# Kernel optimization log

Hardware: AMD Instinct MI355X
Metric: run time of the kernel (lower is better)

## Reference

```python
import jax, jax.numpy as jnp
import numpy as np
from jax import lax

B, T, P, H, O = 64, 96, 256, 128, 24  # batch, seq_len, num_points, hidden_dim, pred_len


def setup_inputs() -> dict:
    key = jax.random.key(0)
    ks = jax.random.split(key, 7)
    s = 1.0 / np.sqrt(H)  # torch LSTM/Linear default init scale
    return {
        "x": jax.random.normal(ks[0], (B, T, P, 1), dtype=jnp.float32),
        "W_ih": jax.random.uniform(ks[1], (P, 4 * H, 1), jnp.float32, -s, s),
        "W_hh": jax.random.uniform(ks[2], (P, 4 * H, H), jnp.float32, -s, s),
        "b_ih": jax.random.uniform(ks[3], (P, 4 * H), jnp.float32, -s, s),
        "b_hh": jax.random.uniform(ks[4], (P, 4 * H), jnp.float32, -s, s),
        "W_fc": jax.random.uniform(ks[5], (P, O, H), jnp.float32, -s, s),
        "b_fc": jax.random.uniform(ks[6], (P, O), jnp.float32, -s, s),
    }


def reference(x, W_ih, W_hh, b_ih, b_hh, W_fc, b_fc):
    # x: [B, T, P, F]; model uses only feature 0
    xs = x[..., 0]  # [B, T, P]
    # input_dim == 1, so input-to-gate contribution is a scaled broadcast of W_ih
    # precompute for all timesteps: [T, B, P, 4H]
    gx = jnp.einsum("btp,pg->tbpg", xs, W_ih[:, :, 0]) + (b_ih + b_hh)

    def step(carry, gxt):
        h, c = carry  # [B, P, H] each
        gates = gxt + jnp.einsum("bph,pgh->bpg", h, W_hh)  # [B, P, 4H]
        i, f, g, o = jnp.split(gates, 4, axis=-1)  # torch gate order i,f,g,o
        i = jax.nn.sigmoid(i)
        f = jax.nn.sigmoid(f)
        g = jnp.tanh(g)
        o = jax.nn.sigmoid(o)
        c = f * c + i * g
        h = o * jnp.tanh(c)
        return (h, c), None

    h0 = jnp.zeros((B, P, H), dtype=x.dtype)
    (h, _), _ = lax.scan(step, (h0, h0), gx)
    # per-point Linear on final hidden state: [B, P, O]
    out = jnp.einsum("bph,poh->bpo", h, W_fc) + b_fc
    # original stacks point outputs on last dim -> [B, pred_len, P]
    return jnp.transpose(out, (0, 2, 1))
```

## Files before the change

kernel.cpp:

```cpp
#include <hip/hip_runtime.h>
#include <hip/hip_bf16.h>

#define Bdim 64
#define Tdim 96
#define Pdim 256
#define Hdim 128
#define Gdim 512
#define Odim 24
#define BH   32

typedef _Float16 f16x8 __attribute__((ext_vector_type(8)));
typedef float    f32x16 __attribute__((ext_vector_type(16)));
typedef float    f32x2  __attribute__((ext_vector_type(2)));

union H8 { uint4 u4; unsigned short s[8]; _Float16 h[8]; f16x8 v; };
union HS { _Float16 h; unsigned short s; };

__device__ __forceinline__ float exp2_fast(float x) {
#if __has_builtin(__builtin_amdgcn_exp2f)
    return __builtin_amdgcn_exp2f(x);
#else
    return __expf(x * 0.6931471805599453f);
#endif
}

__global__ __launch_bounds__(1024, 4)
void lstm_fused(const float* __restrict__ x,
                const float* __restrict__ W_ih,
                const float* __restrict__ W_hh,
                const float* __restrict__ b_ih,
                const float* __restrict__ b_hh,
                const float* __restrict__ W_fc,
                const float* __restrict__ b_fc,
                float* __restrict__ out)
{
    __shared__ unsigned short hb0[2][BH * Hdim];
    __shared__ unsigned short hb1[2][BH * Hdim];

    const int p   = blockIdx.x;
    const int tid = threadIdx.x;
    const int w   = tid >> 6;
    const int l31 = tid & 31;
    const int hi  = (tid >> 5) & 1;

    const float L1 = 1.4426950408889634f;
    const float L2 = 2.0f * L1;

    for (int i = tid; i < 2 * BH * Hdim; i += 1024) ((unsigned short*)hb0)[i] = 0;
    for (int i = tid; i < 2 * BH * Hdim; i += 1024) ((unsigned short*)hb1)[i] = 0;

    f16x8 afr[9];
    {
        const int rp   = w * 32 + l31;
        const int orow = ((rp & 3) << 7) | (rp >> 2);
        const float sc = ((rp & 3) == 2) ? L2 : L1;
        const float* rowp = W_hh + (size_t)p * Gdim * Hdim + (size_t)orow * Hdim;
        #pragma unroll
        for (int ks = 0; ks < 8; ++ks) {
            int k0 = ks * 16 + hi * 8;
            float4 va = *(const float4*)(rowp + k0);
            float4 vb = *(const float4*)(rowp + k0 + 4);
            H8 u;
            u.h[0] = (_Float16)(sc * va.x); u.h[1] = (_Float16)(sc * va.y);
            u.h[2] = (_Float16)(sc * va.z); u.h[3] = (_Float16)(sc * va.w);
            u.h[4] = (_Float16)(sc * vb.x); u.h[5] = (_Float16)(sc * vb.y);
            u.h[6] = (_Float16)(sc * vb.z); u.h[7] = (_Float16)(sc * vb.w);
            afr[ks] = u.v;
        }
        H8 u9;
        #pragma unroll
        for (int j = 0; j < 8; ++j) u9.s[j] = 0;
        if (hi == 0) {
            u9.h[0] = (_Float16)(sc * W_ih[(size_t)p * Gdim + orow]);
            u9.h[1] = (_Float16)(sc * (b_ih[(size_t)p * Gdim + orow] +
                                       b_hh[(size_t)p * Gdim + orow]));
        }
        afr[8] = u9.v;
    }

    auto ldh = [&](const unsigned short* hb, int ks) -> H8 {
        H8 r;
        int c   = ks * 2 + hi;
        int off = (l31 << 8) + ((c ^ (l31 & 15)) << 4);
        r.u4 = *(const uint4*)((const char*)hb + off);
        return r;
    };

    auto ep_pair = [&](const f32x16& a, int j, f32x2* cr, unsigned short* wb) {
        f32x2 yi = {a[8 * j + 0], a[8 * j + 4]};
        f32x2 yf = {a[8 * j + 1], a[8 * j + 5]};
        f32x2 yg = {a[8 * j + 2], a[8 * j + 6]};
        f32x2 yo = {a[8 * j + 3], a[8 * j + 7]};
        f32x2 Ef = {exp2_fast(-yf.x), exp2_fast(-yf.y)};
        f32x2 Ei = {exp2_fast(-yi.x), exp2_fast(-yi.y)};
        f32x2 Eg = {exp2_fast(yg.x),  exp2_fast(yg.y)};
        f32x2 t1 = Ef + 1.0f;
        f32x2 t2 = Ei + 1.0f;
        f32x2 t3 = Eg + 1.0f;
        f32x2 t4 = Eg - 1.0f;
        f32x2 den = (t1 * t2) * t3;
        f32x2 num = (cr[j] * t2) * t3 + (L2 * t4) * t1;
        float D = den.x * den.y;
        float r = __builtin_amdgcn_rcpf(D);
        f32x2 inv = {r * den.y, r * den.x};
        f32x2 cn  = num * inv;
        cn.x = __builtin_amdgcn_fmed3f(cn.x, -30.0f, 30.0f);
        cn.y = __builtin_amdgcn_fmed3f(cn.y, -30.0f, 30.0f);
        cr[j] = cn;
        f32x2 Eo = {exp2_fast(-yo.x), exp2_fast(-yo.y)};
        f32x2 Ec = {exp2_fast(cn.x),  exp2_fast(cn.y)};
        f32x2 d2 = (Eo + 1.0f) * (Ec + 1.0f);
        float D2 = d2.x * d2.y;
        float r2 = __builtin_amdgcn_rcpf(D2);
        f32x2 j2 = {r2 * d2.y, r2 * d2.x};
        f32x2 hv = (Ec - 1.0f) * j2;
        HS ha; ha.h = (_Float16)hv.x;
        HS hc; hc.h = (_Float16)hv.y;
        int base = (l31 << 7) + ((w ^ (l31 & 15)) << 3) + 4 * j + hi;
        wb[base]     = ha.s;
        wb[base + 2] = hc.s;
    };

    auto phase = [&](const unsigned short* rb, unsigned short* wb,
                     f32x16& acc, const f32x16& ar, f32x2* cr, float xv,
                     bool doGemm, bool doEp) {
        if (doGemm) {
            H8 f0 = ldh(rb, 0), f1 = ldh(rb, 1);
            H8 f2 = ldh(rb, 2), f3 = ldh(rb, 3);
            f32x16 z;
            #pragma unroll
            for (int j = 0; j < 16; ++j) z[j] = 0.f;
            acc = __builtin_amdgcn_mfma_f32_32x32x16_f16(afr[0], f0.v, z, 0, 0, 0);
            acc = __builtin_amdgcn_mfma_f32_32x32x16_f16(afr[1], f1.v, acc, 0, 0, 0);
            if (doEp) ep_pair(ar, 0, cr, wb);
            H8 f4 = ldh(rb, 4), f5 = ldh(rb, 5);
            acc = __builtin_amdgcn_mfma_f32_32x32x16_f16(afr[2], f2.v, acc, 0, 0, 0);
            acc = __builtin_amdgcn_mfma_f32_32x32x16_f16(afr[3], f3.v, acc, 0, 0, 0);
            if (doEp) ep_pair(ar, 1, cr, wb);
            H8 f6 = ldh(rb, 6), f7 = ldh(rb, 7);
            acc = __builtin_amdgcn_mfma_f32_32x32x16_f16(afr[4], f4.v, acc, 0, 0, 0);
            acc = __builtin_amdgcn_mfma_f32_32x32x16_f16(afr[5], f5.v, acc, 0, 0, 0);
            acc = __builtin_amdgcn_mfma_f32_32x32x16_f16(afr[6], f6.v, acc, 0, 0, 0);
            acc = __builtin_amdgcn_mfma_f32_32x32x16_f16(afr[7], f7.v, acc, 0, 0, 0);
            H8 bg;
            #pragma unroll
            for (int j = 0; j < 8; ++j) bg.s[j] = 0;
            if (hi == 0) { bg.h[0] = (_Float16)xv; bg.h[1] = (_Float16)1.0f; }
            acc = __builtin_amdgcn_mfma_f32_32x32x16_f16(afr[8], bg.v, acc, 0, 0, 0);
        } else if (doEp) {
            ep_pair(ar, 0, cr, wb);
            ep_pair(ar, 1, cr, wb);
        }
    };

    f32x2 cre0[2] = {f32x2{0.f, 0.f}, f32x2{0.f, 0.f}};
    f32x2 cre1[2] = {f32x2{0.f, 0.f}, f32x2{0.f, 0.f}};
    f32x16 acc0, acc1;
    #pragma unroll
    for (int j = 0; j < 16; ++j) { acc0[j] = 0.f; acc1[j] = 0.f; }

    const float* xp0 = x + (size_t)((0 * BH + l31) * Tdim) * Pdim + p;
    const float* xp1 = x + (size_t)((1 * BH + l31) * Tdim) * Pdim + p;
    float xv0 = xp0[0];
    float xv1 = xp1[0];

    __syncthreads();

    for (int t = 0; t < Tdim; ++t) {
        const int P  = t & 1;
        const int tn = (t + 1 < Tdim) ? (t + 1) : t;
        float xn0 = xp0[(size_t)tn * Pdim];
        float xn1 = xp1[(size_t)tn * Pdim];

        phase(hb0[P], hb0[P ^ 1], acc0, acc1, cre1, xv0, true, false);
        phase(hb1[P], hb0[P ^ 1], acc1, acc0, cre0, xv1, true, true);
        phase(hb1[P], hb1[P ^ 1], acc1, acc1, cre1, 0.f, false, true);

        __syncthreads();
        xv0 = xn0;
        xv1 = xn1;
    }

    const float* wfc = W_fc + (size_t)p * Odim * Hdim;
    const float* bfc = b_fc + (size_t)p * Odim;
    for (int i = tid; i < Bdim * Odim; i += 1024) {
        int o = i % Odim;
        int b = i / Odim;
        int bl = (b < BH) ? b : (b - BH);
        const unsigned short* hr = (b < BH) ? (hb0[0] + (bl << 7))
                                            : (hb1[0] + (bl << 7));
        float s = bfc[o];
        const float* wr = wfc + o * Hdim;
        #pragma unroll 8
        for (int k2 = 0; k2 < Hdim; ++k2) {
            int idx = (((k2 >> 3) ^ (bl & 15)) << 3) + (k2 & 7);
            HS s2; s2.s = hr[idx];
            s = __builtin_fmaf(wr[k2], (float)s2.h, s);
        }
        out[(size_t)b * Odim * Pdim + (size_t)o * Pdim + p] = s;
    }
}

extern "C" void kernel_launch(void* const* d_in, const int* in_sizes, int n_in,
                              void* d_out, int out_size, void* d_ws, size_t ws_size,
                              hipStream_t stream) {
    const float* x    = (const float*)d_in[0];
    const float* W_ih = (const float*)d_in[1];
    const float* W_hh = (const float*)d_in[2];
    const float* b_ih = (const float*)d_in[3];
    const float* b_hh = (const float*)d_in[4];
    const float* W_fc = (const float*)d_in[5];
    const float* b_fc = (const float*)d_in[6];
    float* out = (float*)d_out;

    lstm_fused<<<dim3(Pdim), dim3(1024), 0, stream>>>(x, W_ih, W_hh, b_ih, b_hh, W_fc, b_fc, out);
}
```

Before: 390.3 us.

## Split batch halves across separate blocks instead of interleaving within one block

Before, each block handled one point and both 32-row batch halves, interleaving the GEMM of one half with the gate epilogue of the other to hide latency. Now the grid has 512 blocks, each running one batch half for one point, with half the shared memory and a straight GEMM-then-epilogue step. This gives more blocks for the 256 CUs and lowers register/LDS pressure. In exchange it loses the in-block overlap of MFMA and transcendental work, and each W_hh slice is loaded and converted twice.

```diff
diff --git a/kernel.cpp b/kernel.cpp
--- a/kernel.cpp
+++ b/kernel.cpp
@@ -24,7 +24,7 @@
 #endif
 }
 
-__global__ __launch_bounds__(1024, 4)
+__global__ __launch_bounds__(1024, 8)
 void lstm_fused(const float* __restrict__ x,
                 const float* __restrict__ W_ih,
                 const float* __restrict__ W_hh,
@@ -34,10 +34,11 @@
                 const float* __restrict__ b_fc,
                 float* __restrict__ out)
 {
-    __shared__ unsigned short hb0[2][BH * Hdim];
-    __shared__ unsigned short hb1[2][BH * Hdim];
+    __shared__ unsigned short hb[2][BH * Hdim];
 
-    const int p   = blockIdx.x;
+    const int bid = blockIdx.x;
+    const int p   = bid & 255;
+    const int s   = bid >> 8;
     const int tid = threadIdx.x;
     const int w   = tid >> 6;
     const int l31 = tid & 31;
@@ -46,10 +47,10 @@
     const float L1 = 1.4426950408889634f;
     const float L2 = 2.0f * L1;
 
-    for (int i = tid; i < 2 * BH * Hdim; i += 1024) ((unsigned short*)hb0)[i] = 0;
-    for (int i = tid; i < 2 * BH * Hdim; i += 1024) ((unsigned short*)hb1)[i] = 0;
+    for (int i = tid; i < 2 * BH * Hdim; i += 1024) ((unsigned short*)hb)[i] = 0;
 
-    f16x8 afr[9];
+    f16x8 afr[8];
+    unsigned int wb9;
     {
         const int rp   = w * 32 + l31;
         const int orow = ((rp & 3) << 7) | (rp >> 2);
@@ -67,22 +68,17 @@
             u.h[6] = (_Float16)(sc * vb.z); u.h[7] = (_Float16)(sc * vb.w);
             afr[ks] = u.v;
         }
-        H8 u9;
-        #pragma unroll
-        for (int j = 0; j < 8; ++j) u9.s[j] = 0;
-        if (hi == 0) {
-            u9.h[0] = (_Float16)(sc * W_ih[(size_t)p * Gdim + orow]);
-            u9.h[1] = (_Float16)(sc * (b_ih[(size_t)p * Gdim + orow] +
+        HS t0; t0.h = (_Float16)(sc * W_ih[(size_t)p * Gdim + orow]);
+        HS t1; t1.h = (_Float16)(sc * (b_ih[(size_t)p * Gdim + orow] +
                                        b_hh[(size_t)p * Gdim + orow]));
-        }
-        afr[8] = u9.v;
+        wb9 = (hi == 0) ? ((unsigned)t0.s | ((unsigned)t1.s << 16)) : 0u;
     }
 
-    auto ldh = [&](const unsigned short* hb, int ks) -> H8 {
+    auto ldh = [&](const unsigned short* rb, int ks) -> H8 {
         H8 r;
         int c   = ks * 2 + hi;
         int off = (l31 << 8) + ((c ^ (l31 & 15)) << 4);
-        r.u4 = *(const uint4*)((const char*)hb + off);
+        r.u4 = *(const uint4*)((const char*)rb + off);
         return r;
     };
 
@@ -121,83 +117,67 @@
         wb[base + 2] = hc.s;
     };
 
-    auto phase = [&](const unsigned short* rb, unsigned short* wb,
-                     f32x16& acc, const f32x16& ar, f32x2* cr, float xv,
-                     bool doGemm, bool doEp) {
-        if (doGemm) {
-            H8 f0 = ldh(rb, 0), f1 = ldh(rb, 1);
-            H8 f2 = ldh(rb, 2), f3 = ldh(rb, 3);
-            f32x16 z;
-            #pragma unroll
-            for (int j = 0; j < 16; ++j) z[j] = 0.f;
-            acc = __builtin_amdgcn_mfma_f32_32x32x16_f16(afr[0], f0.v, z, 0, 0, 0);
-            acc = __builtin_amdgcn_mfma_f32_32x32x16_f16(afr[1], f1.v, acc, 0, 0, 0);
-            if (doEp) ep_pair(ar, 0, cr, wb);
-            H8 f4 = ldh(rb, 4), f5 = ldh(rb, 5);
-            acc = __builtin_amdgcn_mfma_f32_32x32x16_f16(afr[2], f2.v, acc, 0, 0, 0);
-            acc = __builtin_amdgcn_mfma_f32_32x32x16_f16(afr[3], f3.v, acc, 0, 0, 0);
-            if (doEp) ep_pair(ar, 1, cr, wb);
-            H8 f6 = ldh(rb, 6), f7 = ldh(rb, 7);
-            acc = __builtin_amdgcn_mfma_f32_32x32x16_f16(afr[4], f4.v, acc, 0, 0, 0);
-            acc = __builtin_amdgcn_mfma_f32_32x32x16_f16(afr[5], f5.v, acc, 0, 0, 0);
-            acc = __builtin_amdgcn_mfma_f32_32x32x16_f16(afr[6], f6.v, acc, 0, 0, 0);
-            acc = __builtin_amdgcn_mfma_f32_32x32x16_f16(afr[7], f7.v, acc, 0, 0, 0);
-            H8 bg;
-            #pragma unroll
-            for (int j = 0; j < 8; ++j) bg.s[j] = 0;
-            if (hi == 0) { bg.h[0] = (_Float16)xv; bg.h[1] = (_Float16)1.0f; }
-            acc = __builtin_amdgcn_mfma_f32_32x32x16_f16(afr[8], bg.v, acc, 0, 0, 0);
-        } else if (doEp) {
-            ep_pair(ar, 0, cr, wb);
-            ep_pair(ar, 1, cr, wb);
-        }
-    };
+    f32x2 cre[2] = {f32x2{0.f, 0.f}, f32x2{0.f, 0.f}};
 
-    f32x2 cre0[2] = {f32x2{0.f, 0.f}, f32x2{0.f, 0.f}};
-    f32x2 cre1[2] = {f32x2{0.f, 0.f}, f32x2{0.f, 0.f}};
-    f32x16 acc0, acc1;
-    #pragma unroll
-    for (int j = 0; j < 16; ++j) { acc0[j] = 0.f; acc1[j] = 0.f; }
-
-    const float* xp0 = x + (size_t)((0 * BH + l31) * Tdim) * Pdim + p;
-    const float* xp1 = x + (size_t)((1 * BH + l31) * Tdim) * Pdim + p;
-    float xv0 = xp0[0];
-    float xv1 = xp1[0];
+    const float* xp = x + (size_t)((s * BH + l31) * Tdim) * Pdim + p;
+    float xv = xp[0];
 
     __syncthreads();
 
     for (int t = 0; t < Tdim; ++t) {
         const int P  = t & 1;
+        const unsigned short* rb = hb[P];
+        unsigned short*       wb = hb[P ^ 1];
         const int tn = (t + 1 < Tdim) ? (t + 1) : t;
-        float xn0 = xp0[(size_t)tn * Pdim];
-        float xn1 = xp1[(size_t)tn * Pdim];
+        float xn = xp[(size_t)tn * Pdim];
 
-        phase(hb0[P], hb0[P ^ 1], acc0, acc1, cre1, xv0, true, false);
-        phase(hb1[P], hb0[P ^ 1], acc1, acc0, cre0, xv1, true, true);
-        phase(hb1[P], hb1[P ^ 1], acc1, acc1, cre1, 0.f, false, true);
+        f32x16 acc;
+        {
+            H8 f0 = ldh(rb, 0), f1 = ldh(rb, 1);
+            f32x16 z;
+            #pragma unroll
+            for (int j = 0; j < 16; ++j) z[j] = 0.f;
+            acc = __builtin_amdgcn_mfma_f32_32x32x16_f16(afr[0], f0.v, z, 0, 0, 0);
+            H8 f2 = ldh(rb, 2), f3 = ldh(rb, 3);
+            acc = __builtin_amdgcn_mfma_f32_32x32x16_f16(afr[1], f1.v, acc, 0, 0, 0);
+            acc = __builtin_amdgcn_mfma_f32_32x32x16_f16(afr[2], f2.v, acc, 0, 0, 0);
+            H8 f4 = ldh(rb, 4), f5 = ldh(rb, 5);
+            acc = __builtin_amdgcn_mfma_f32_32x32x16_f16(afr[3], f3.v, acc, 0, 0, 0);
+            acc = __builtin_amdgcn_mfma_f32_32x32x16_f16(afr[4], f4.v, acc, 0, 0, 0);
+            H8 f6 = ldh(rb, 6), f7 = ldh(rb, 7);
+            acc = __builtin_amdgcn_mfma_f32_32x32x16_f16(afr[5], f5.v, acc, 0, 0, 0);
+            acc = __builtin_amdgcn_mfma_f32_32x32x16_f16(afr[6], f6.v, acc, 0, 0, 0);
+            acc = __builtin_amdgcn_mfma_f32_32x32x16_f16(afr[7], f7.v, acc, 0, 0, 0);
+            H8 a9; a9.u4.x = wb9; a9.u4.y = 0; a9.u4.z = 0; a9.u4.w = 0;
+            HS bx; bx.h = (_Float16)xv;
+            H8 bg; bg.u4.x = (hi == 0) ? ((unsigned)bx.s | (0x3C00u << 16)) : 0u;
+            bg.u4.y = 0; bg.u4.z = 0; bg.u4.w = 0;
+            acc = __builtin_amdgcn_mfma_f32_32x32x16_f16(a9.v, bg.v, acc, 0, 0, 0);
+        }
+
+        ep_pair(acc, 0, cre, wb);
+        ep_pair(acc, 1, cre, wb);
 
         __syncthreads();
-        xv0 = xn0;
-        xv1 = xn1;
+        xv = xn;
     }
 
     const float* wfc = W_fc + (size_t)p * Odim * Hdim;
     const float* bfc = b_fc + (size_t)p * Odim;
-    for (int i = tid; i < Bdim * Odim; i += 1024) {
-        int o = i % Odim;
-        int b = i / Odim;
-        int bl = (b < BH) ? b : (b - BH);
-        const unsigned short* hr = (b < BH) ? (hb0[0] + (bl << 7))
-                                            : (hb1[0] + (bl << 7));
-        float s = bfc[o];
+    for (int i = tid; i < BH * Odim; i += 1024) {
+        int o  = i % Odim;
+        int bl = i / Odim;
+        int b  = s * BH + bl;
+        const unsigned short* hr = hb[0] + (bl << 7);
+        float sum = bfc[o];
         const float* wr = wfc + o * Hdim;
         #pragma unroll 8
         for (int k2 = 0; k2 < Hdim; ++k2) {
             int idx = (((k2 >> 3) ^ (bl & 15)) << 3) + (k2 & 7);
             HS s2; s2.s = hr[idx];
-            s = __builtin_fmaf(wr[k2], (float)s2.h, s);
+            sum = __builtin_fmaf(wr[k2], (float)s2.h, sum);
         }
-        out[(size_t)b * Odim * Pdim + (size_t)o * Pdim + p] = s;
+        out[(size_t)b * Odim * Pdim + (size_t)o * Pdim + p] = sum;
     }
 }
 
@@ -213,5 +193,5 @@
     const float* b_fc = (const float*)d_in[6];
     float* out = (float*)d_out;
 
-    lstm_fused<<<dim3(Pdim), dim3(1024), 0, stream>>>(x, W_ih, W_hh, b_ih, b_hh, W_fc, b_fc, out);
+    lstm_fused<<<dim3(2 * Pdim), dim3(1024), 0, stream>>>(x, W_ih, W_hh, b_ih, b_hh, W_fc, b_fc, out);
 }
```

After: 672.5 us. 1.72x slower.
